# Performance work log

Measured on AMD Instinct MI355X. Metric: run time of the kernel, lower is better.

Reference implementation:

```python
import jax, jax.numpy as jnp
import numpy as np

EPS = 1e-12  # F.normalize default eps


def setup_inputs() -> dict:
    key = jax.random.key(0)
    k1, k2 = jax.random.split(key)
    x = jax.random.normal(k1, (2, 96, 48, 48, 48), dtype=jnp.float32)  # backbone features [B,C,D,H,W]
    prototypes = jax.random.normal(k2, (512, 96), dtype=jnp.float32)   # nn.Parameter(512, 96)
    return {"x": x, "prototypes": prototypes}


def reference(x, prototypes):
    # F.normalize(x, dim=1): divide by max(||x||_2, eps) along channel dim
    xn = x / jnp.maximum(jnp.linalg.norm(x, axis=1, keepdims=True), EPS)
    xn = jnp.moveaxis(xn, 1, -1)  # [B, D, H, W, C]
    # F.normalize(prototypes, dim=1)
    pn = prototypes / jnp.maximum(jnp.linalg.norm(prototypes, axis=1, keepdims=True), EPS)
    # cosine similarity against all prototypes: [B, D, H, W, K]
    sims = jnp.einsum("bdhwc,kc->bdhwk", xn, pn)
    return jnp.argmax(sims, axis=-1)  # [B, D, H, W] int
```

## Files before the change

### kernel.cpp

```cpp
#include <hip/hip_runtime.h>
#include <math.h>

#define C 96
#define K 512
#define P_PER_B 110592
#define NPOS 221184
#define MT 32
#define ITERS_SIM 4
#define GRID_SIM 1728
#define XROW 104


typedef _Float16 f16;
typedef _Float16 f16x8 __attribute__((ext_vector_type(8)));
typedef float f32x4 __attribute__((ext_vector_type(4)));


__global__ __launch_bounds__(256) void prep_kernel(const float* __restrict__ proto,
                                                   float* __restrict__ pnT,
                                                   f16* __restrict__ pn16h,
                                                   f16* __restrict__ pn16l) {
    int k = blockIdx.x * 256 + threadIdx.x;
    if (k >= K) return;
    const float* row = proto + k * C;
    float r[8];
#pragma unroll
    for (int j = 0; j < 8; ++j) r[j] = __fmul_rn(row[j], row[j]);
    for (int i = 8; i < C; i += 8) {
#pragma unroll
        for (int j = 0; j < 8; ++j)
            r[j] = __fadd_rn(r[j], __fmul_rn(row[i + j], row[i + j]));
    }
    float res = __fadd_rn(__fadd_rn(__fadd_rn(r[0], r[1]), __fadd_rn(r[2], r[3])),
                          __fadd_rn(__fadd_rn(r[4], r[5]), __fadd_rn(r[6], r[7])));
    float n = fmaxf(__fsqrt_rn(res), 1e-12f);
    for (int c = 0; c < C; ++c) {
        float v = __fdiv_rn(row[c], n);
        pnT[(size_t)c * K + k] = v;
        f16 h = (f16)v;
        pn16h[(size_t)k * C + c] = h;
        pn16l[(size_t)k * C + c] = (f16)(v - (float)h);
    }
}

__global__ __launch_bounds__(1024, 4) void sim_argmax_kernel(
        const float* __restrict__ x,
        const f16* __restrict__ pn16h,
        const f16* __restrict__ pn16l,
        int* __restrict__ out) {
    __shared__ __align__(16) f16 xth[MT * XROW];
    __shared__ __align__(16) f16 xtl[MT * XROW];
    __shared__ float n2p[32][MT];
    __shared__ float wm1[16][MT], wm2[16][MT];

    const int tid = threadIdx.x;
    const int lane = tid & 63;
    const int w = tid >> 6;
    const int l15 = lane & 15;
    const int lg = lane >> 4;
    const int lg4 = lg << 2;

    f16x8 afh[2][3], afl[2][3];
#pragma unroll
    for (int t = 0; t < 2; ++t)
#pragma unroll
        for (int q = 0; q < 3; ++q) {
            size_t off = (size_t)(w * 32 + t * 16 + l15) * C + q * 32 + lg * 8;
            afh[t][q] = *(const f16x8*)(pn16h + off);
            afl[t][q] = *(const f16x8*)(pn16l + off);
        }

    const int pos_s = tid & 31;
    const int cg = tid >> 5;

    const int m00 = blockIdx.x * (MT * ITERS_SIM);
    const int b = (m00 >= P_PER_B) ? 1 : 0;
    const float* xq = x + (size_t)b * (size_t)C * P_PER_B + (m00 - b * P_PER_B)
                    + (size_t)(cg * 3) * P_PER_B + pos_s;

    float fl[3];
#pragma unroll
    for (int j = 0; j < 3; ++j) fl[j] = xq[(size_t)j * P_PER_B];

#pragma unroll 1
    for (int it = 0; it < ITERS_SIM; ++it) {
        const int m0 = m00 + it * MT;

        __syncthreads();

        float ss = 0.f;
#pragma unroll
        for (int j = 0; j < 3; ++j) {
            float v = fl[j];
            ss = fmaf(v, v, ss);
            f16 h = (f16)v;
            xth[pos_s * XROW + cg * 3 + j] = h;
            xtl[pos_s * XROW + cg * 3 + j] = (f16)(v - (float)h);
        }
        n2p[cg][pos_s] = ss;
        __syncthreads();

        if (it != ITERS_SIM - 1) {
#pragma unroll
            for (int j = 0; j < 3; ++j)
                fl[j] = xq[(size_t)j * P_PER_B + (it + 1) * MT];
        }

        f32x4 acc[2][2];
#pragma unroll
        for (int s = 0; s < 2; ++s)
#pragma unroll
            for (int t = 0; t < 2; ++t)
                acc[s][t] = (f32x4){0.f, 0.f, 0.f, 0.f};
#pragma unroll
        for (int q = 0; q < 3; ++q) {
            const int co = q * 32 + lg * 8;
            f16x8 b0h = *(const f16x8*)(xth + l15 * XROW + co);
            f16x8 b1h = *(const f16x8*)(xth + (16 + l15) * XROW + co);
            f16x8 b0l = *(const f16x8*)(xtl + l15 * XROW + co);
            f16x8 b1l = *(const f16x8*)(xtl + (16 + l15) * XROW + co);
#pragma unroll
            for (int t = 0; t < 2; ++t) {
                acc[0][t] = __builtin_amdgcn_mfma_f32_16x16x32_f16(afh[t][q], b0h, acc[0][t], 0, 0, 0);
                acc[0][t] = __builtin_amdgcn_mfma_f32_16x16x32_f16(afh[t][q], b0l, acc[0][t], 0, 0, 0);
                acc[0][t] = __builtin_amdgcn_mfma_f32_16x16x32_f16(afl[t][q], b0h, acc[0][t], 0, 0, 0);
                acc[1][t] = __builtin_amdgcn_mfma_f32_16x16x32_f16(afh[t][q], b1h, acc[1][t], 0, 0, 0);
                acc[1][t] = __builtin_amdgcn_mfma_f32_16x16x32_f16(afh[t][q], b1l, acc[1][t], 0, 0, 0);
                acc[1][t] = __builtin_amdgcn_mfma_f32_16x16x32_f16(afl[t][q], b1h, acc[1][t], 0, 0, 0);
            }
        }

        float m1[2], m2[2];
        m1[0] = m1[1] = -3.4e38f;
        m2[0] = m2[1] = -3.4e38f;
        const int kb = w * 32 + lg4;
#pragma unroll
        for (int t = 0; t < 2; ++t)
#pragma unroll
            for (int r = 0; r < 4; ++r) {
                const int kk = kb + t * 16 + r;
#pragma unroll
                for (int s = 0; s < 2; ++s) {
                    float pk = __uint_as_float(
                        (__float_as_uint(acc[s][t][r]) & 0xFFFFFE00u) | (unsigned)kk);
                    m2[s] = fmaxf(m2[s], fminf(m1[s], pk));
                    m1[s] = fmaxf(m1[s], pk);
                }
            }

#pragma unroll
        for (int m = 16; m <= 32; m <<= 1)
#pragma unroll
            for (int s = 0; s < 2; ++s) {
                float o1 = __shfl_xor(m1[s], m);
                float o2 = __shfl_xor(m2[s], m);
                m2[s] = fmaxf(fmaxf(m2[s], o2), fminf(m1[s], o1));
                m1[s] = fmaxf(m1[s], o1);
            }
        if (lane < 16) {
            wm1[w][l15] = m1[0];      wm2[w][l15] = m2[0];
            wm1[w][16 + l15] = m1[1]; wm2[w][16 + l15] = m2[1];
        }
        __syncthreads();

        if (tid < MT) {
            float n2 = 0.f;
#pragma unroll
            for (int g = 0; g < 32; ++g) n2 += n2p[g][tid];
            float b_ = wm1[0][tid], s_ = wm2[0][tid];
#pragma unroll
            for (int ww = 1; ww < 16; ++ww) {
                float o1 = wm1[ww][tid], o2 = wm2[ww][tid];
                s_ = fmaxf(fmaxf(s_, o2), fminf(b_, o1));
                b_ = fmaxf(b_, o1);
            }
            float tau = 2.6e-4f * sqrtf(n2) + 3e-5f;
            int k_ = (int)(__float_as_uint(b_) & 511u);
            out[m0 + tid] = (b_ - s_ < tau) ? (k_ | (int)0x80000000) : k_;
        }
    }
}

__global__ __launch_bounds__(256) void refine_kernel(
        const float* __restrict__ x,
        const float* __restrict__ pnT,
        int* __restrict__ out) {
    __shared__ int list[MT];
    __shared__ int cnt;
    __shared__ float xn[C];
    __shared__ float nrm_s;
    __shared__ float sval[4];
    __shared__ int sidx[4];

    int tid = threadIdx.x;

    if (tid == 0) cnt = 0;
    __syncthreads();

    if (tid < MT) {
        int g = blockIdx.x * MT + tid;
        if (out[g] < 0) {
            int i = atomicAdd(&cnt, 1);
            list[i] = g;
        }
    }
    __syncthreads();
    int n = cnt;

    for (int i = 0; i < n; ++i) {
        int gg = list[i];
        int b = (gg >= P_PER_B) ? 1 : 0;
        int p = gg - b * P_PER_B;
        const float* xb = x + (size_t)b * (size_t)C * P_PER_B + p;

        if (tid < C) xn[tid] = xb[(size_t)tid * P_PER_B];
        __syncthreads();

        if (tid == 0) {
            float acc = __fmul_rn(xn[0], xn[0]);
            for (int c = 1; c < C; ++c)
                acc = __fadd_rn(acc, __fmul_rn(xn[c], xn[c]));
            nrm_s = fmaxf(__fsqrt_rn(acc), 1e-12f);
        }
        __syncthreads();
        if (tid < C) xn[tid] = __fdiv_rn(xn[tid], nrm_s);
        __syncthreads();

        float s0 = 0.f, s1 = 0.f;
        for (int c = 0; c < C; ++c) {
            s0 = __fadd_rn(s0, __fmul_rn(xn[c], pnT[(size_t)c * K + tid]));
            s1 = __fadd_rn(s1, __fmul_rn(xn[c], pnT[(size_t)c * K + tid + 256]));
        }

        float bv = s0;
        int bk = tid;
        if (s1 > bv) { bv = s1; bk = tid + 256; }

#pragma unroll
        for (int off = 1; off < 64; off <<= 1) {
            float ov = __shfl_xor(bv, off);
            int oi = __shfl_xor(bk, off);
            if (ov > bv || (ov == bv && oi < bk)) { bv = ov; bk = oi; }
        }
        int wv = tid >> 6;
        if ((tid & 63) == 0) { sval[wv] = bv; sidx[wv] = bk; }
        __syncthreads();

        if (tid == 0) {
            float fb = sval[0];
            int fk = sidx[0];
            for (int ww = 1; ww < 4; ++ww) {
                if (sval[ww] > fb || (sval[ww] == fb && sidx[ww] < fk)) {
                    fb = sval[ww]; fk = sidx[ww];
                }
            }
            out[gg] = fk;
        }
        __syncthreads();
    }
}

extern "C" void kernel_launch(void* const* d_in, const int* in_sizes, int n_in,
                              void* d_out, int out_size, void* d_ws, size_t ws_size,
                              hipStream_t stream) {
    const float* x = (const float*)d_in[0];
    const float* proto = (const float*)d_in[1];
    int* out = (int*)d_out;

    float* pnT = (float*)d_ws;
    f16* pn16h = (f16*)((char*)d_ws + 196608);
    f16* pn16l = (f16*)((char*)d_ws + 294912);

    prep_kernel<<<2, 256, 0, stream>>>(proto, pnT, pn16h, pn16l);
    sim_argmax_kernel<<<GRID_SIM, 1024, 0, stream>>>(x, pn16h, pn16l, out);
    refine_kernel<<<NPOS / MT, 256, 0, stream>>>(x, pnT, out);
}
```

Measured before the change: 265.2 us.

## Widen sim tile to 64 positions with channel-blocked LDS and parallel refine

```diff
diff --git a/kernel.cpp b/kernel.cpp
--- a/kernel.cpp
+++ b/kernel.cpp
@@ -5,10 +5,10 @@
 #define K 512
 #define P_PER_B 110592
 #define NPOS 221184
-#define MT 32
-#define ITERS_SIM 4
+#define MT 64
+#define ITERS_SIM 2
 #define GRID_SIM 1728
-#define XROW 104
+#define CB 12
 
 
 typedef _Float16 f16;
@@ -48,9 +48,9 @@
         const f16* __restrict__ pn16h,
         const f16* __restrict__ pn16l,
         int* __restrict__ out) {
-    __shared__ __align__(16) f16 xth[MT * XROW];
-    __shared__ __align__(16) f16 xtl[MT * XROW];
-    __shared__ float n2p[32][MT];
+    __shared__ __align__(16) f16 xth[CB * MT * 8];
+    __shared__ __align__(16) f16 xtl[CB * MT * 8];
+    __shared__ float n2p[CB][MT];
     __shared__ float wm1[16][MT], wm2[16][MT];
 
     const int tid = threadIdx.x;
@@ -58,7 +58,6 @@
     const int w = tid >> 6;
     const int l15 = lane & 15;
     const int lg = lane >> 4;
-    const int lg4 = lg << 2;
 
     f16x8 afh[2][3], afl[2][3];
 #pragma unroll
@@ -70,79 +69,84 @@
             afl[t][q] = *(const f16x8*)(pn16l + off);
         }
 
-    const int pos_s = tid & 31;
-    const int cg = tid >> 5;
-
     const int m00 = blockIdx.x * (MT * ITERS_SIM);
     const int b = (m00 >= P_PER_B) ? 1 : 0;
     const float* xq = x + (size_t)b * (size_t)C * P_PER_B + (m00 - b * P_PER_B)
-                    + (size_t)(cg * 3) * P_PER_B + pos_s;
-
-    float fl[3];
-#pragma unroll
-    for (int j = 0; j < 3; ++j) fl[j] = xq[(size_t)j * P_PER_B];
-
-#pragma unroll 1
+                    + (size_t)(w << 3) * P_PER_B + lane;
+
+#pragma unroll
     for (int it = 0; it < ITERS_SIM; ++it) {
         const int m0 = m00 + it * MT;
 
         __syncthreads();
 
-        float ss = 0.f;
-#pragma unroll
-        for (int j = 0; j < 3; ++j) {
-            float v = fl[j];
-            ss = fmaf(v, v, ss);
-            f16 h = (f16)v;
-            xth[pos_s * XROW + cg * 3 + j] = h;
-            xtl[pos_s * XROW + cg * 3 + j] = (f16)(v - (float)h);
-        }
-        n2p[cg][pos_s] = ss;
-        __syncthreads();
-
-        if (it != ITERS_SIM - 1) {
-#pragma unroll
-            for (int j = 0; j < 3; ++j)
-                fl[j] = xq[(size_t)j * P_PER_B + (it + 1) * MT];
-        }
-
-        f32x4 acc[2][2];
-#pragma unroll
-        for (int s = 0; s < 2; ++s)
+        if (w < CB) {
+            float ss = 0.f;
+            f16x8 vh, vl;
+#pragma unroll
+            for (int j = 0; j < 8; ++j) {
+                float v = xq[(size_t)j * P_PER_B + it * MT];
+                ss = fmaf(v, v, ss);
+                f16 h = (f16)v;
+                vh[j] = h;
+                vl[j] = (f16)(v - (float)h);
+            }
+            n2p[w][lane] = ss;
+            *(f16x8*)(xth + ((w * MT + lane) << 3)) = vh;
+            *(f16x8*)(xtl + ((w * MT + lane) << 3)) = vl;
+        }
+        __syncthreads();
+
+        f32x4 acc[4][2];
+#pragma unroll
+        for (int s = 0; s < 4; ++s)
 #pragma unroll
             for (int t = 0; t < 2; ++t)
                 acc[s][t] = (f32x4){0.f, 0.f, 0.f, 0.f};
 #pragma unroll
         for (int q = 0; q < 3; ++q) {
-            const int co = q * 32 + lg * 8;
-            f16x8 b0h = *(const f16x8*)(xth + l15 * XROW + co);
-            f16x8 b1h = *(const f16x8*)(xth + (16 + l15) * XROW + co);
-            f16x8 b0l = *(const f16x8*)(xtl + l15 * XROW + co);
-            f16x8 b1l = *(const f16x8*)(xtl + (16 + l15) * XROW + co);
-#pragma unroll
-            for (int t = 0; t < 2; ++t) {
-                acc[0][t] = __builtin_amdgcn_mfma_f32_16x16x32_f16(afh[t][q], b0h, acc[0][t], 0, 0, 0);
-                acc[0][t] = __builtin_amdgcn_mfma_f32_16x16x32_f16(afh[t][q], b0l, acc[0][t], 0, 0, 0);
-                acc[0][t] = __builtin_amdgcn_mfma_f32_16x16x32_f16(afl[t][q], b0h, acc[0][t], 0, 0, 0);
-                acc[1][t] = __builtin_amdgcn_mfma_f32_16x16x32_f16(afh[t][q], b1h, acc[1][t], 0, 0, 0);
-                acc[1][t] = __builtin_amdgcn_mfma_f32_16x16x32_f16(afh[t][q], b1l, acc[1][t], 0, 0, 0);
-                acc[1][t] = __builtin_amdgcn_mfma_f32_16x16x32_f16(afl[t][q], b1h, acc[1][t], 0, 0, 0);
-            }
-        }
-
-        float m1[2], m2[2];
-        m1[0] = m1[1] = -3.4e38f;
-        m2[0] = m2[1] = -3.4e38f;
-        const int kb = w * 32 + lg4;
+            const int cbase = ((q * 4 + lg) * MT) << 3;
+            f16x8 bh[4], bl[4];
+#pragma unroll
+            for (int s = 0; s < 4; ++s)
+                bh[s] = *(const f16x8*)(xth + cbase + ((s * 16 + l15) << 3));
+#pragma unroll
+            for (int s = 0; s < 4; ++s)
+#pragma unroll
+                for (int t = 0; t < 2; ++t)
+                    acc[s][t] = __builtin_amdgcn_mfma_f32_16x16x32_f16(
+                        afh[t][q], bh[s], acc[s][t], 0, 0, 0);
+#pragma unroll
+            for (int s = 0; s < 4; ++s)
+                bl[s] = *(const f16x8*)(xtl + cbase + ((s * 16 + l15) << 3));
+#pragma unroll
+            for (int s = 0; s < 4; ++s)
+#pragma unroll
+                for (int t = 0; t < 2; ++t)
+                    acc[s][t] = __builtin_amdgcn_mfma_f32_16x16x32_f16(
+                        afl[t][q], bh[s], acc[s][t], 0, 0, 0);
+#pragma unroll
+            for (int s = 0; s < 4; ++s)
+#pragma unroll
+                for (int t = 0; t < 2; ++t)
+                    acc[s][t] = __builtin_amdgcn_mfma_f32_16x16x32_f16(
+                        afh[t][q], bl[s], acc[s][t], 0, 0, 0);
+        }
+
+        float m1[4], m2[4];
+#pragma unroll
+        for (int s = 0; s < 4; ++s) { m1[s] = -3.4e38f; m2[s] = -3.4e38f; }
+        const int kb = w * 32 + (lg << 2);
 #pragma unroll
         for (int t = 0; t < 2; ++t)
 #pragma unroll
             for (int r = 0; r < 4; ++r) {
                 const int kk = kb + t * 16 + r;
 #pragma unroll
-                for (int s = 0; s < 2; ++s) {
+                for (int s = 0; s < 4; ++s) {
+                    float v = acc[s][t][r];
                     float pk = __uint_as_float(
-                        (__float_as_uint(acc[s][t][r]) & 0xFFFFFE00u) | (unsigned)kk);
+                        (__float_as_uint(v) & 0xFFFFFE00u) | (unsigned)kk);
                     m2[s] = fmaxf(m2[s], fminf(m1[s], pk));
                     m1[s] = fmaxf(m1[s], pk);
                 }
@@ -151,22 +155,25 @@
 #pragma unroll
         for (int m = 16; m <= 32; m <<= 1)
 #pragma unroll
-            for (int s = 0; s < 2; ++s) {
+            for (int s = 0; s < 4; ++s) {
                 float o1 = __shfl_xor(m1[s], m);
                 float o2 = __shfl_xor(m2[s], m);
                 m2[s] = fmaxf(fmaxf(m2[s], o2), fminf(m1[s], o1));
                 m1[s] = fmaxf(m1[s], o1);
             }
         if (lane < 16) {
-            wm1[w][l15] = m1[0];      wm2[w][l15] = m2[0];
-            wm1[w][16 + l15] = m1[1]; wm2[w][16 + l15] = m2[1];
+#pragma unroll
+            for (int s = 0; s < 4; ++s) {
+                wm1[w][s * 16 + l15] = m1[s];
+                wm2[w][s * 16 + l15] = m2[s];
+            }
         }
         __syncthreads();
 
         if (tid < MT) {
             float n2 = 0.f;
 #pragma unroll
-            for (int g = 0; g < 32; ++g) n2 += n2p[g][tid];
+            for (int g = 0; g < CB; ++g) n2 += n2p[g][tid];
             float b_ = wm1[0][tid], s_ = wm2[0][tid];
 #pragma unroll
             for (int ww = 1; ww < 16; ++ww) {
@@ -185,78 +192,82 @@
         const float* __restrict__ x,
         const float* __restrict__ pnT,
         int* __restrict__ out) {
-    __shared__ int list[MT];
+    __shared__ int list[32];
     __shared__ int cnt;
-    __shared__ float xn[C];
-    __shared__ float nrm_s;
-    __shared__ float sval[4];
-    __shared__ int sidx[4];
-
-    int tid = threadIdx.x;
+    __shared__ float xn4[4][C];
+    __shared__ float nrm4[4];
+
+    const int tid = threadIdx.x;
+    const int lane = tid & 63;
+    const int w = tid >> 6;
 
     if (tid == 0) cnt = 0;
     __syncthreads();
 
-    if (tid < MT) {
-        int g = blockIdx.x * MT + tid;
+    if (tid < 32) {
+        int g = blockIdx.x * 32 + tid;
         if (out[g] < 0) {
             int i = atomicAdd(&cnt, 1);
             list[i] = g;
         }
     }
     __syncthreads();
-    int n = cnt;
-
-    for (int i = 0; i < n; ++i) {
-        int gg = list[i];
-        int b = (gg >= P_PER_B) ? 1 : 0;
-        int p = gg - b * P_PER_B;
+    const int n = cnt;
+    const int nmax = (n + 3) >> 2;
+
+    for (int j = 0; j < nmax; ++j) {
+        const int idx = j * 4 + w;
+        const bool act = idx < n;
+        const int gg = act ? list[idx] : list[0];
+        const int b = (gg >= P_PER_B) ? 1 : 0;
+        const int p = gg - b * P_PER_B;
         const float* xb = x + (size_t)b * (size_t)C * P_PER_B + p;
 
-        if (tid < C) xn[tid] = xb[(size_t)tid * P_PER_B];
-        __syncthreads();
-
-        if (tid == 0) {
-            float acc = __fmul_rn(xn[0], xn[0]);
+        if (act) {
+            xn4[w][lane] = xb[(size_t)lane * P_PER_B];
+            if (lane < C - 64) xn4[w][64 + lane] = xb[(size_t)(64 + lane) * P_PER_B];
+        }
+        __syncthreads();
+
+        if (act && lane == 0) {
+            float a = __fmul_rn(xn4[w][0], xn4[w][0]);
             for (int c = 1; c < C; ++c)
-                acc = __fadd_rn(acc, __fmul_rn(xn[c], xn[c]));
-            nrm_s = fmaxf(__fsqrt_rn(acc), 1e-12f);
-        }
-        __syncthreads();
-        if (tid < C) xn[tid] = __fdiv_rn(xn[tid], nrm_s);
-        __syncthreads();
-
-        float s0 = 0.f, s1 = 0.f;
-        for (int c = 0; c < C; ++c) {
-            s0 = __fadd_rn(s0, __fmul_rn(xn[c], pnT[(size_t)c * K + tid]));
-            s1 = __fadd_rn(s1, __fmul_rn(xn[c], pnT[(size_t)c * K + tid + 256]));
-        }
-
-        float bv = s0;
-        int bk = tid;
-        if (s1 > bv) { bv = s1; bk = tid + 256; }
-
-#pragma unroll
-        for (int off = 1; off < 64; off <<= 1) {
-            float ov = __shfl_xor(bv, off);
-            int oi = __shfl_xor(bk, off);
-            if (ov > bv || (ov == bv && oi < bk)) { bv = ov; bk = oi; }
-        }
-        int wv = tid >> 6;
-        if ((tid & 63) == 0) { sval[wv] = bv; sidx[wv] = bk; }
-        __syncthreads();
-
-        if (tid == 0) {
-            float fb = sval[0];
-            int fk = sidx[0];
-            for (int ww = 1; ww < 4; ++ww) {
-                if (sval[ww] > fb || (sval[ww] == fb && sidx[ww] < fk)) {
-                    fb = sval[ww]; fk = sidx[ww];
-                }
-            }
-            out[gg] = fk;
-        }
-        __syncthreads();
+                a = __fadd_rn(a, __fmul_rn(xn4[w][c], xn4[w][c]));
+            nrm4[w] = fmaxf(__fsqrt_rn(a), 1e-12f);
+        }
+        __syncthreads();
+        if (act) {
+            xn4[w][lane] = __fdiv_rn(xn4[w][lane], nrm4[w]);
+            if (lane < C - 64)
+                xn4[w][64 + lane] = __fdiv_rn(xn4[w][64 + lane], nrm4[w]);
+        }
+        __syncthreads();
+
+        if (act) {
+            float s[8];
+#pragma unroll
+            for (int r = 0; r < 8; ++r) s[r] = 0.f;
+            for (int c = 0; c < C; ++c) {
+                float xc = xn4[w][c];
+                const float* pr = pnT + (size_t)c * K + lane;
+#pragma unroll
+                for (int r = 0; r < 8; ++r)
+                    s[r] = __fadd_rn(s[r], __fmul_rn(xc, pr[r * 64]));
+            }
+            float bv = s[0];
+            int bk = lane;
+#pragma unroll
+            for (int r = 1; r < 8; ++r) {
+                if (s[r] > bv) { bv = s[r]; bk = lane + r * 64; }
+            }
+#pragma unroll
+            for (int off = 1; off < 64; off <<= 1) {
+                float ov = __shfl_xor(bv, off);
+                int oi = __shfl_xor(bk, off);
+                if (ov > bv || (ov == bv && oi < bk)) { bv = ov; bk = oi; }
+            }
+            if (lane == 0) out[gg] = bk;
+        }
     }
 }
 
@@ -273,5 +284,5 @@
 
     prep_kernel<<<2, 256, 0, stream>>>(proto, pnT, pn16h, pn16l);
     sim_argmax_kernel<<<GRID_SIM, 1024, 0, stream>>>(x, pn16h, pn16l, out);
-    refine_kernel<<<NPOS / MT, 256, 0, stream>>>(x, pnT, out);
-}
+    refine_kernel<<<NPOS / 32, 256, 0, stream>>>(x, pnT, out);
+}
```

Measured after the change: 253.3 us. 4.5% less time.
